# Performance work log

Measured on AMD Instinct MI355X. Metric: run time of the kernel, lower is better.

The kernel has to match this reference:

```python
import jax, jax.numpy as jnp
import numpy as np

# Model dims
B, S, D = 1, 768, 256          # batch, seq_len, d_model
H, KD = 8, 256                 # num_heads, key_dim
DH = KD // H                   # head_dim = 32
BS, NR, W, G = 64, 3, 3, 1     # block_size, num_rand_blocks, window_size, global_tokens
NEG = -1e9


def _build_sparse_indices(seed=0):
    """Replicates _create_sparse_attention_mask (sparse branch) with numpy.
    Returns (attn_indices [S, M] int32 clamped >=0, blocked_mask [1,1,S,M] float32)."""
    nb = S // BS  # num_blocks (S divisible by BS here)
    rng = np.random.RandomState(seed)
    r = np.arange(nb)
    # window pairs |i - j| <= W
    ii, jj = np.meshgrid(r, r, indexing='ij')
    win = np.abs(ii - jj) <= W
    window_pairs = np.stack([ii[win], jj[win]], axis=1)
    # global: every block -> first G blocks; first G blocks -> every block
    g = np.arange(G)
    glob_to = np.stack([np.repeat(r, G), np.tile(g, nb)], axis=1)
    glob_from = np.stack([np.repeat(g, nb), np.tile(r, G)], axis=1)
    # random pairs
    rand_pairs = rng.randint(0, nb, size=(NR * nb, 2))
    allp = np.concatenate([window_pairs, glob_to, glob_from, rand_pairs], axis=0)
    uniq = np.unique(allp[:, 0] * nb + allp[:, 1])  # sorted unique (row, col)
    rows, cols = uniq // nb, uniq % nb
    max_row = int(np.max(np.bincount(rows, minlength=nb)))
    M = max_row * BS  # padded neighbor-token width (= S when a global block is dense)
    idx = np.full((nb, M), -1, dtype=np.int64)
    for b in range(nb):
        cs = cols[rows == b]
        toks = (cs[:, None] * BS + np.arange(BS)[None, :]).reshape(-1)
        idx[b, :toks.size] = toks
    tok_idx = idx[np.arange(S) // BS]  # expand per-block rows to per-token rows [S, M]
    mask = np.where(tok_idx >= 0, 0.0, NEG).astype(np.float32)
    return np.maximum(tok_idx, 0).astype(np.int32), mask[None, None]


def setup_inputs() -> dict:
    key = jax.random.key(0)
    ks = jax.random.split(key, 8)

    def dense_w(k, fi, fo):  # glorot-uniform like keras Dense
        lim = float(np.sqrt(6.0 / (fi + fo)))
        return jax.random.uniform(k, (fi, fo), jnp.float32, -lim, lim)

    attn_indices, blocked_mask = _build_sparse_indices()
    return {
        'query': jax.random.normal(ks[0], (B, S, D), jnp.float32),
        'value': jax.random.normal(ks[1], (B, S, D), jnp.float32),
        'key_in': jax.random.normal(ks[2], (B, S, D), jnp.float32),
        'Wq': dense_w(ks[3], D, KD), 'bq': jnp.zeros((KD,), jnp.float32),
        'Wk': dense_w(ks[4], D, KD), 'bk': jnp.zeros((KD,), jnp.float32),
        'Wv': dense_w(ks[5], D, KD), 'bv': jnp.zeros((KD,), jnp.float32),
        'Wo': dense_w(ks[6], KD, D), 'bo': jnp.zeros((D,), jnp.float32),
        'attn_indices': jnp.asarray(attn_indices),
        'blocked_mask': jnp.asarray(blocked_mask),
    }


def reference(query, value, key_in, Wq, bq, Wk, bk, Wv, bv, Wo, bo, attn_indices, blocked_mask):
    q = query @ Wq + bq
    k = key_in @ Wk + bk
    v = value @ Wv + bv

    def split_heads(x):  # [B,S,KD] -> [B*H,S,DH]
        return x.reshape(B, S, H, DH).transpose(0, 2, 1, 3).reshape(B * H, S, DH)

    q = split_heads(q) * (DH ** -0.5)
    k = split_heads(k)
    v = split_heads(v)

    # gather sparse neighbor tokens (indices shared across batch*heads)
    k_g = jnp.take(k, attn_indices, axis=1)  # [BH, S, M, DH]
    v_g = jnp.take(v, attn_indices, axis=1)  # [BH, S, M, DH]

    scores = jnp.einsum('bnd,bnmd->bnm', q, k_g)  # [BH, S, M]
    M = attn_indices.shape[1]
    scores = scores.reshape(B, H, S, M) + blocked_mask  # pad positions -> -1e9
    probs = jax.nn.softmax(scores, axis=-1)

    ctx = jnp.einsum('bnm,bnmd->bnd', probs.reshape(B * H, S, M), v_g)  # [BH,S,DH]
    ctx = ctx.reshape(B, H, S, DH).transpose(0, 2, 1, 3).reshape(B, S, KD)
    out = ctx @ Wo + bo
    return out, scores, attn_indices
```

## Files before the change

### kernel.cpp

```cpp
#include <hip/hip_runtime.h>
#include <math.h>

#define SQ 768
#define DMODEL 256
#define NH 8
#define DHD 32
#define NB 12
#define QSCALE 0.1767766952966369f
#define PSHIFT 8.0f

__global__ __launch_bounds__(256) void proj3(
    const float* __restrict__ query, const float* __restrict__ value,
    const float* __restrict__ key_in,
    const float* __restrict__ Wq, const float* __restrict__ bq,
    const float* __restrict__ Wk, const float* __restrict__ bk,
    const float* __restrict__ Wv, const float* __restrict__ bv,
    const float* __restrict__ bo, float* __restrict__ outbuf,
    const int* __restrict__ aidx, float* __restrict__ idx_out,
    float* __restrict__ qhp, float* __restrict__ khp, float* __restrict__ vhp)
{
    const int j = threadIdx.x;

    {
        const int bidf = blockIdx.y * 96 + blockIdx.x;
        const int i0 = (bidf * 256 + j) * 8;
        int4 a = *(const int4*)&aidx[i0];
        int4 b = *(const int4*)&aidx[i0 + 4];
        *(float4*)&idx_out[i0] =
            make_float4((float)a.x, (float)a.y, (float)a.z, (float)a.w);
        *(float4*)&idx_out[i0 + 4] =
            make_float4((float)b.x, (float)b.y, (float)b.z, (float)b.w);
    }

    const int s0 = blockIdx.x * 8;
    const int w  = blockIdx.y;

    if (w == 0) {
        const float bb = bo[j];
        #pragma unroll
        for (int r = 0; r < 8; ++r)
            outbuf[(s0 + r) * DMODEL + j] = bb;
    }

    const float *X, *W, *bias; float* outp; float scale;
    if (w == 0)      { X = query;  W = Wq; bias = bq; outp = qhp; scale = QSCALE; }
    else if (w == 1) { X = key_in; W = Wk; bias = bk; outp = khp; scale = 1.0f; }
    else             { X = value;  W = Wv; bias = bv; outp = vhp; scale = 1.0f; }

    __shared__ __align__(16) float xs[8][DMODEL];
    __shared__ __align__(16) float ws[2][32 * DMODEL];

    {
        float* xsf = &xs[0][0];
        const float* Xp = X + s0 * DMODEL;
        const int i0 = j * 8;
        *(float4*)&xsf[i0]     = *(const float4*)&Xp[i0];
        *(float4*)&xsf[i0 + 4] = *(const float4*)&Xp[i0 + 4];

        #pragma unroll
        for (int t = 0; t < 8; ++t)
            *(float4*)&ws[0][t * 1024 + j * 4] =
                *(const float4*)&W[t * 1024 + j * 4];
    }
    __syncthreads();

    const int j0 = (j & 63) * 4;
    const int r0 = (j >> 6) * 2;

    float4 acc0 = make_float4(0.f, 0.f, 0.f, 0.f);
    float4 acc1 = make_float4(0.f, 0.f, 0.f, 0.f);
    int cur = 0;

    for (int c = 0; c < 8; ++c) {
        float4 wreg[8];
        if (c < 7) {
            const float* Wc = W + (c + 1) * 8192;
            #pragma unroll
            for (int t = 0; t < 8; ++t)
                wreg[t] = *(const float4*)&Wc[t * 1024 + j * 4];
        }

        const float* wb = &ws[cur][0];
        #pragma unroll
        for (int k4 = 0; k4 < 8; ++k4) {
            const int kb = c * 32 + k4 * 4;
            float4 x0 = *(const float4*)&xs[r0 + 0][kb];
            float4 x1 = *(const float4*)&xs[r0 + 1][kb];
            float4 w0 = *(const float4*)&wb[(k4 * 4 + 0) * DMODEL + j0];
            float4 w1 = *(const float4*)&wb[(k4 * 4 + 1) * DMODEL + j0];
            float4 w2 = *(const float4*)&wb[(k4 * 4 + 2) * DMODEL + j0];
            float4 w3 = *(const float4*)&wb[(k4 * 4 + 3) * DMODEL + j0];
            acc0.x = fmaf(x0.x, w0.x, acc0.x); acc0.y = fmaf(x0.x, w0.y, acc0.y);
            acc0.z = fmaf(x0.x, w0.z, acc0.z); acc0.w = fmaf(x0.x, w0.w, acc0.w);
            acc0.x = fmaf(x0.y, w1.x, acc0.x); acc0.y = fmaf(x0.y, w1.y, acc0.y);
            acc0.z = fmaf(x0.y, w1.z, acc0.z); acc0.w = fmaf(x0.y, w1.w, acc0.w);
            acc0.x = fmaf(x0.z, w2.x, acc0.x); acc0.y = fmaf(x0.z, w2.y, acc0.y);
            acc0.z = fmaf(x0.z, w2.z, acc0.z); acc0.w = fmaf(x0.z, w2.w, acc0.w);
            acc0.x = fmaf(x0.w, w3.x, acc0.x); acc0.y = fmaf(x0.w, w3.y, acc0.y);
            acc0.z = fmaf(x0.w, w3.z, acc0.z); acc0.w = fmaf(x0.w, w3.w, acc0.w);
            acc1.x = fmaf(x1.x, w0.x, acc1.x); acc1.y = fmaf(x1.x, w0.y, acc1.y);
            acc1.z = fmaf(x1.x, w0.z, acc1.z); acc1.w = fmaf(x1.x, w0.w, acc1.w);
            acc1.x = fmaf(x1.y, w1.x, acc1.x); acc1.y = fmaf(x1.y, w1.y, acc1.y);
            acc1.z = fmaf(x1.y, w1.z, acc1.z); acc1.w = fmaf(x1.y, w1.w, acc1.w);
            acc1.x = fmaf(x1.z, w2.x, acc1.x); acc1.y = fmaf(x1.z, w2.y, acc1.y);
            acc1.z = fmaf(x1.z, w2.z, acc1.z); acc1.w = fmaf(x1.z, w2.w, acc1.w);
            acc1.x = fmaf(x1.w, w3.x, acc1.x); acc1.y = fmaf(x1.w, w3.y, acc1.y);
            acc1.z = fmaf(x1.w, w3.z, acc1.z); acc1.w = fmaf(x1.w, w3.w, acc1.w);
        }

        if (c < 7) {
            float* wd = &ws[cur ^ 1][0];
            #pragma unroll
            for (int t = 0; t < 8; ++t)
                *(float4*)&wd[t * 1024 + j * 4] = wreg[t];
            __syncthreads();
            cur ^= 1;
        }
    }

    const float4 bb = *(const float4*)&bias[j0];
    const int h = j0 >> 5, d = j0 & 31;
    {
        float4 o0, o1;
        o0.x = (acc0.x + bb.x) * scale; o0.y = (acc0.y + bb.y) * scale;
        o0.z = (acc0.z + bb.z) * scale; o0.w = (acc0.w + bb.w) * scale;
        o1.x = (acc1.x + bb.x) * scale; o1.y = (acc1.y + bb.y) * scale;
        o1.z = (acc1.z + bb.z) * scale; o1.w = (acc1.w + bb.w) * scale;
        *(float4*)&outp[h * (SQ * DHD) + (s0 + r0 + 0) * DHD + d] = o0;
        *(float4*)&outp[h * (SQ * DHD) + (s0 + r0 + 1) * DHD + d] = o1;
    }
}

__global__ __launch_bounds__(512) void attn2(
    const float* __restrict__ qh, const float* __restrict__ kh,
    const float* __restrict__ vh, const int* __restrict__ aidx,
    const float* __restrict__ mask, const float* __restrict__ Wo,
    float* __restrict__ scores_out, float* __restrict__ out, int M)
{
    __shared__ __align__(16) float Ks[2][2][32][68];
    __shared__ __align__(16) float Vs[2][2][64][36];
    __shared__ __align__(16) float Ps[2][32][68];
    __shared__ float dot0s[32];
    __shared__ float invL[32];

    const int b    = blockIdx.x;
    const int half = blockIdx.y;
    const int h    = blockIdx.z;
    const int s0b  = b * 64;
    const int s0   = s0b + half * 32;
    const int tid  = threadIdx.x;
    const int u    = tid >> 8;
    const int utid = tid & 255;
    const int NCH2 = M / 128;

    const int qrt = (utid & 15) * 2;
    const int qct = (utid >> 4) * 4;
    const int rp  = utid & 15;
    const int dg  = (utid >> 4) & 3;
    const int cg  = utid >> 6;
    const int c   = utid & 63;
    const int sg  = utid >> 6;
    const int d4a = sg * 4;
    const int d4b = 16 + sg * 4;

    const float* mrow = &mask[s0b * M];
    const int*   arow = &aidx[s0b * M];
    float*       srow = &scores_out[(h * SQ + s0) * M];

    float qr0[32], qr1[32];
    {
        const float* qp = &qh[(h * SQ + s0 + qrt) * DHD];
        #pragma unroll
        for (int d4 = 0; d4 < DHD; d4 += 4) {
            float4 a  = *(const float4*)&qp[d4];
            float4 b4 = *(const float4*)&qp[DHD + d4];
            qr0[d4] = a.x;  qr0[d4+1] = a.y;  qr0[d4+2] = a.z;  qr0[d4+3] = a.w;
            qr1[d4] = b4.x; qr1[d4+1] = b4.y; qr1[d4+2] = b4.z; qr1[d4+3] = b4.w;
        }
    }

    if (tid < 16) {
        const float* k0 = &kh[h * SQ * DHD];
        float a0 = 0.f, a1 = 0.f;
        #pragma unroll
        for (int d = 0; d < DHD; ++d) {
            const float kv = k0[d];
            a0 = fmaf(qr0[d], kv, a0);
            a1 = fmaf(qr1[d], kv, a1);
        }
        dot0s[qrt] = a0; dot0s[qrt + 1] = a1;
    }

    float mv_cur = mrow[(u * NCH2) * 64];
    bool  val_cur = mv_cur > -0.5f;
    if (val_cur) {
        const int t0 = arow[(u * NCH2) * 64];
        const float* kp = &kh[(h * SQ + t0 + c) * DHD];
        const float* vp = &vh[(h * SQ + t0 + c) * DHD];
        float4 ka = *(const float4*)&kp[d4a];
        float4 kb = *(const float4*)&kp[d4b];
        Ks[u][0][d4a+0][c] = ka.x; Ks[u][0][d4a+1][c] = ka.y;
        Ks[u][0][d4a+2][c] = ka.z; Ks[u][0][d4a+3][c] = ka.w;
        Ks[u][0][d4b+0][c] = kb.x; Ks[u][0][d4b+1][c] = kb.y;
        Ks[u][0][d4b+2][c] = kb.z; Ks[u][0][d4b+3][c] = kb.w;
        *(float4*)&Vs[u][0][c][d4a] = *(const float4*)&vp[d4a];
        *(float4*)&Vs[u][0][c][d4b] = *(const float4*)&vp[d4b];
    }
    __syncthreads();

    float4 acc0a = make_float4(0.f,0.f,0.f,0.f), acc0b = acc0a;
    float4 acc1a = acc0a, acc1b = acc0a;
    float rps0 = 0.f, rps1 = 0.f;
    int cur = 0;

    for (int ci = 0; ci < NCH2; ++ci) {
        const int m0 = (u * NCH2 + ci) * 64;

        bool  val_nxt = false;
        float mv_nxt  = 0.f;
        float4 ka, kb, va, vb;
        if (ci + 1 < NCH2) {
            mv_nxt  = mrow[m0 + 64];
            val_nxt = mv_nxt > -0.5f;
            if (val_nxt) {
                const int t0 = arow[m0 + 64];
                const float* kp = &kh[(h * SQ + t0 + c) * DHD];
                const float* vp = &vh[(h * SQ + t0 + c) * DHD];
                ka = *(const float4*)&kp[d4a];
                kb = *(const float4*)&kp[d4b];
                va = *(const float4*)&vp[d4a];
                vb = *(const float4*)&vp[d4b];
            }
        }

        if (val_cur) {
            const float* Kb = &Ks[u][cur][0][qct];
            float sc[2][4] = {};
            #pragma unroll
            for (int kk = 0; kk < 32; ++kk) {
                float4 b4 = *(const float4*)&Kb[kk * 68];
                sc[0][0] = fmaf(qr0[kk], b4.x, sc[0][0]);
                sc[0][1] = fmaf(qr0[kk], b4.y, sc[0][1]);
                sc[0][2] = fmaf(qr0[kk], b4.z, sc[0][2]);
                sc[0][3] = fmaf(qr0[kk], b4.w, sc[0][3]);
                sc[1][0] = fmaf(qr1[kk], b4.x, sc[1][0]);
                sc[1][1] = fmaf(qr1[kk], b4.y, sc[1][1]);
                sc[1][2] = fmaf(qr1[kk], b4.z, sc[1][2]);
                sc[1][3] = fmaf(qr1[kk], b4.w, sc[1][3]);
            }
            {
                *(float4*)&srow[(qrt + 0) * M + m0 + qct] =
                    make_float4(sc[0][0], sc[0][1], sc[0][2], sc[0][3]);
                float4 e;
                e.x = __expf(sc[0][0] - PSHIFT); e.y = __expf(sc[0][1] - PSHIFT);
                e.z = __expf(sc[0][2] - PSHIFT); e.w = __expf(sc[0][3] - PSHIFT);
                *(float4*)&Ps[u][qrt + 0][qct] = e;
                rps0 += (e.x + e.y) + (e.z + e.w);
            }
            {
                *(float4*)&srow[(qrt + 1) * M + m0 + qct] =
                    make_float4(sc[1][0], sc[1][1], sc[1][2], sc[1][3]);
                float4 e;
                e.x = __expf(sc[1][0] - PSHIFT); e.y = __expf(sc[1][1] - PSHIFT);
                e.z = __expf(sc[1][2] - PSHIFT); e.w = __expf(sc[1][3] - PSHIFT);
                *(float4*)&Ps[u][qrt + 1][qct] = e;
                rps1 += (e.x + e.y) + (e.z + e.w);
            }
        } else {
            #pragma unroll
            for (int i = 0; i < 8; ++i) {
                const int e = utid + i * 256;
                const int r = e >> 6, cc = e & 63;
                srow[r * M + m0 + cc] = dot0s[r] + mv_cur;
            }
        }

        if (val_nxt) {
            Ks[u][cur^1][d4a+0][c] = ka.x; Ks[u][cur^1][d4a+1][c] = ka.y;
            Ks[u][cur^1][d4a+2][c] = ka.z; Ks[u][cur^1][d4a+3][c] = ka.w;
            Ks[u][cur^1][d4b+0][c] = kb.x; Ks[u][cur^1][d4b+1][c] = kb.y;
            Ks[u][cur^1][d4b+2][c] = kb.z; Ks[u][cur^1][d4b+3][c] = kb.w;
            *(float4*)&Vs[u][cur^1][c][d4a] = va;
            *(float4*)&Vs[u][cur^1][c][d4b] = vb;
        }
        __syncthreads();

        if (val_cur) {
            const float (*Vb)[36] = Vs[u][cur];
            const float* Pr0 = &Ps[u][2 * rp][0];
            const float* Pr1 = &Ps[u][2 * rp + 1][0];
            const int c0 = cg * 16;
            const int dd = dg * 8;
            #pragma unroll
            for (int k = 0; k < 4; ++k) {
                float4 pa = *(const float4*)&Pr0[c0 + k * 4];
                float4 pb = *(const float4*)&Pr1[c0 + k * 4];
                const float pav[4] = {pa.x, pa.y, pa.z, pa.w};
                const float pbv[4] = {pb.x, pb.y, pb.z, pb.w};
                #pragma unroll
                for (int t = 0; t < 4; ++t) {
                    const int cc2 = c0 + k * 4 + t;
                    float4 v0 = *(const float4*)&Vb[cc2][dd];
                    float4 v1 = *(const float4*)&Vb[cc2][dd + 4];
                    acc0a.x = fmaf(pav[t], v0.x, acc0a.x);
                    acc0a.y = fmaf(pav[t], v0.y, acc0a.y);
                    acc0a.z = fmaf(pav[t], v0.z, acc0a.z);
                    acc0a.w = fmaf(pav[t], v0.w, acc0a.w);
                    acc0b.x = fmaf(pav[t], v1.x, acc0b.x);
                    acc0b.y = fmaf(pav[t], v1.y, acc0b.y);
                    acc0b.z = fmaf(pav[t], v1.z, acc0b.z);
                    acc0b.w = fmaf(pav[t], v1.w, acc0b.w);
                    acc1a.x = fmaf(pbv[t], v0.x, acc1a.x);
                    acc1a.y = fmaf(pbv[t], v0.y, acc1a.y);
                    acc1a.z = fmaf(pbv[t], v0.z, acc1a.z);
                    acc1a.w = fmaf(pbv[t], v0.w, acc1a.w);
                    acc1b.x = fmaf(pbv[t], v1.x, acc1b.x);
                    acc1b.y = fmaf(pbv[t], v1.y, acc1b.y);
                    acc1b.z = fmaf(pbv[t], v1.z, acc1b.z);
                    acc1b.w = fmaf(pbv[t], v1.w, acc1b.w);
                }
            }
        }
        __syncthreads();

        val_cur = val_nxt; mv_cur = mv_nxt; cur ^= 1;
    }

    float* vacc = &Vs[0][0][0][0];
    float* rsum = &Ps[0][0][0];
    {
        const int s = u * 4 + cg;
        float* base = vacc + (s * 32 + 2 * rp) * 36 + dg * 8;
        *(float4*)&base[0]  = acc0a; *(float4*)&base[4]  = acc0b;
        *(float4*)&base[36] = acc1a; *(float4*)&base[40] = acc1b;
        const int qg = utid >> 4;
        rsum[(u * 16 + qg) * 32 + qrt]     = rps0;
        rsum[(u * 16 + qg) * 32 + qrt + 1] = rps1;
    }
    __syncthreads();

    if (tid < 32) {
        float pt = 0.f;
        #pragma unroll
        for (int s2 = 0; s2 < 32; ++s2) pt += rsum[s2 * 32 + tid];
        invL[tid] = 1.0f / pt;
    }
    __syncthreads();

    float* ctxn = &Ks[0][0][0][0];
    if (tid < 256) {
        const int r = tid & 31, dq = tid >> 5;
        float4 sum = make_float4(0.f, 0.f, 0.f, 0.f);
        #pragma unroll
        for (int s = 0; s < 8; ++s) {
            float4 v = *(const float4*)&vacc[(s * 32 + r) * 36 + dq * 4];
            sum.x += v.x; sum.y += v.y; sum.z += v.z; sum.w += v.w;
        }
        const float il = invL[r];
        sum.x *= il; sum.y *= il; sum.z *= il; sum.w *= il;
        *(float4*)&ctxn[r * 36 + dq * 4] = sum;
    }
    __syncthreads();

    {
        const int jc = tid & 255, rg = tid >> 8;
        float wo[32];
        #pragma unroll
        for (int k = 0; k < 32; ++k)
            wo[k] = Wo[(h * DHD + k) * DMODEL + jc];
        for (int rr = rg * 16; rr < rg * 16 + 16; ++rr) {
            float a = 0.f;
            #pragma unroll
            for (int k4 = 0; k4 < 8; ++k4) {
                float4 cv = *(const float4*)&ctxn[rr * 36 + k4 * 4];
                a = fmaf(cv.x, wo[k4 * 4 + 0], a);
                a = fmaf(cv.y, wo[k4 * 4 + 1], a);
                a = fmaf(cv.z, wo[k4 * 4 + 2], a);
                a = fmaf(cv.w, wo[k4 * 4 + 3], a);
            }
            atomicAdd(&out[(s0 + rr) * DMODEL + jc], a);
        }
    }
}

extern "C" void kernel_launch(void* const* d_in, const int* in_sizes, int n_in,
                              void* d_out, int out_size, void* d_ws, size_t ws_size,
                              hipStream_t stream)
{
    const float* query  = (const float*)d_in[0];
    const float* value  = (const float*)d_in[1];
    const float* key_in = (const float*)d_in[2];
    const float* Wq = (const float*)d_in[3];
    const float* bq = (const float*)d_in[4];
    const float* Wk = (const float*)d_in[5];
    const float* bk = (const float*)d_in[6];
    const float* Wv = (const float*)d_in[7];
    const float* bv = (const float*)d_in[8];
    const float* Wo = (const float*)d_in[9];
    const float* bo = (const float*)d_in[10];
    const int*   aidx = (const int*)d_in[11];
    const float* mask = (const float*)d_in[12];

    const int M = in_sizes[11] / SQ;

    float* out        = (float*)d_out;
    float* scores_out = out + SQ * DMODEL;
    float* idx_out    = scores_out + NH * SQ * M;

    float* ws  = (float*)d_ws;
    float* qhp = ws;
    float* khp = qhp + NH * SQ * DHD;
    float* vhp = khp + NH * SQ * DHD;

    proj3<<<dim3(96, 3), 256, 0, stream>>>(
        query, value, key_in, Wq, bq, Wk, bk, Wv, bv,
        bo, out, aidx, idx_out, qhp, khp, vhp);

    attn2<<<dim3(NB, 2, NH), 512, 0, stream>>>(
        qhp, khp, vhp, aidx, mask, Wo, scores_out, out, M);
}
```

Baseline: 48.88 us.

## Fuse P·V into the score loop using transposed V and register accumulators

V tiles are now stored transposed in shared memory, and each thread multiplies its own exponentiated scores by V right after computing them. This drops the shared-memory probability buffer and one block barrier per chunk. Partial context sums are then reduced across lanes with warp shuffles before the final cross-wave reduction. In exchange each thread holds 64 float accumulators plus the q registers, which raises register pressure and may lower occupancy. The transposed V stores are scalar writes.

```diff
diff --git a/kernel.cpp b/kernel.cpp
--- a/kernel.cpp
+++ b/kernel.cpp
@@ -138,8 +138,7 @@
     float* __restrict__ scores_out, float* __restrict__ out, int M)
 {
     __shared__ __align__(16) float Ks[2][2][32][68];
-    __shared__ __align__(16) float Vs[2][2][64][36];
-    __shared__ __align__(16) float Ps[2][32][68];
+    __shared__ __align__(16) float Vt[2][2][32][68];
     __shared__ float dot0s[32];
     __shared__ float invL[32];
 
@@ -155,9 +154,6 @@
 
     const int qrt = (utid & 15) * 2;
     const int qct = (utid >> 4) * 4;
-    const int rp  = utid & 15;
-    const int dg  = (utid >> 4) & 3;
-    const int cg  = utid >> 6;
     const int c   = utid & 63;
     const int sg  = utid >> 6;
     const int d4a = sg * 4;
@@ -199,17 +195,22 @@
         const float* vp = &vh[(h * SQ + t0 + c) * DHD];
         float4 ka = *(const float4*)&kp[d4a];
         float4 kb = *(const float4*)&kp[d4b];
+        float4 va = *(const float4*)&vp[d4a];
+        float4 vb = *(const float4*)&vp[d4b];
         Ks[u][0][d4a+0][c] = ka.x; Ks[u][0][d4a+1][c] = ka.y;
         Ks[u][0][d4a+2][c] = ka.z; Ks[u][0][d4a+3][c] = ka.w;
         Ks[u][0][d4b+0][c] = kb.x; Ks[u][0][d4b+1][c] = kb.y;
         Ks[u][0][d4b+2][c] = kb.z; Ks[u][0][d4b+3][c] = kb.w;
-        *(float4*)&Vs[u][0][c][d4a] = *(const float4*)&vp[d4a];
-        *(float4*)&Vs[u][0][c][d4b] = *(const float4*)&vp[d4b];
+        Vt[u][0][d4a+0][c] = va.x; Vt[u][0][d4a+1][c] = va.y;
+        Vt[u][0][d4a+2][c] = va.z; Vt[u][0][d4a+3][c] = va.w;
+        Vt[u][0][d4b+0][c] = vb.x; Vt[u][0][d4b+1][c] = vb.y;
+        Vt[u][0][d4b+2][c] = vb.z; Vt[u][0][d4b+3][c] = vb.w;
     }
     __syncthreads();
 
-    float4 acc0a = make_float4(0.f,0.f,0.f,0.f), acc0b = acc0a;
-    float4 acc1a = acc0a, acc1b = acc0a;
+    float a0s[32], a1s[32];
+    #pragma unroll
+    for (int d = 0; d < 32; ++d) { a0s[d] = 0.f; a1s[d] = 0.f; }
     float rps0 = 0.f, rps1 = 0.f;
     int cur = 0;
 
@@ -248,23 +249,27 @@
                 sc[1][2] = fmaf(qr1[kk], b4.z, sc[1][2]);
                 sc[1][3] = fmaf(qr1[kk], b4.w, sc[1][3]);
             }
-            {
-                *(float4*)&srow[(qrt + 0) * M + m0 + qct] =
-                    make_float4(sc[0][0], sc[0][1], sc[0][2], sc[0][3]);
-                float4 e;
-                e.x = __expf(sc[0][0] - PSHIFT); e.y = __expf(sc[0][1] - PSHIFT);
-                e.z = __expf(sc[0][2] - PSHIFT); e.w = __expf(sc[0][3] - PSHIFT);
-                *(float4*)&Ps[u][qrt + 0][qct] = e;
-                rps0 += (e.x + e.y) + (e.z + e.w);
-            }
-            {
-                *(float4*)&srow[(qrt + 1) * M + m0 + qct] =
-                    make_float4(sc[1][0], sc[1][1], sc[1][2], sc[1][3]);
-                float4 e;
-                e.x = __expf(sc[1][0] - PSHIFT); e.y = __expf(sc[1][1] - PSHIFT);
-                e.z = __expf(sc[1][2] - PSHIFT); e.w = __expf(sc[1][3] - PSHIFT);
-                *(float4*)&Ps[u][qrt + 1][qct] = e;
-                rps1 += (e.x + e.y) + (e.z + e.w);
+            *(float4*)&srow[(qrt + 0) * M + m0 + qct] =
+                make_float4(sc[0][0], sc[0][1], sc[0][2], sc[0][3]);
+            *(float4*)&srow[(qrt + 1) * M + m0 + qct] =
+                make_float4(sc[1][0], sc[1][1], sc[1][2], sc[1][3]);
+            float e0[4], e1[4];
+            #pragma unroll
+            for (int t = 0; t < 4; ++t) {
+                e0[t] = __expf(sc[0][t] - PSHIFT);
+                e1[t] = __expf(sc[1][t] - PSHIFT);
+            }
+            rps0 += (e0[0] + e0[1]) + (e0[2] + e0[3]);
+            rps1 += (e1[0] + e1[1]) + (e1[2] + e1[3]);
+
+            const float* Vb = &Vt[u][cur][0][qct];
+            #pragma unroll
+            for (int d = 0; d < 32; ++d) {
+                float4 v = *(const float4*)&Vb[d * 68];
+                a0s[d] = fmaf(e0[0], v.x, fmaf(e0[1], v.y,
+                         fmaf(e0[2], v.z, fmaf(e0[3], v.w, a0s[d]))));
+                a1s[d] = fmaf(e1[0], v.x, fmaf(e1[1], v.y,
+                         fmaf(e1[2], v.z, fmaf(e1[3], v.w, a1s[d]))));
             }
         } else {
             #pragma unroll
@@ -280,74 +285,53 @@
             Ks[u][cur^1][d4a+2][c] = ka.z; Ks[u][cur^1][d4a+3][c] = ka.w;
             Ks[u][cur^1][d4b+0][c] = kb.x; Ks[u][cur^1][d4b+1][c] = kb.y;
             Ks[u][cur^1][d4b+2][c] = kb.z; Ks[u][cur^1][d4b+3][c] = kb.w;
-            *(float4*)&Vs[u][cur^1][c][d4a] = va;
-            *(float4*)&Vs[u][cur^1][c][d4b] = vb;
+            Vt[u][cur^1][d4a+0][c] = va.x; Vt[u][cur^1][d4a+1][c] = va.y;
+            Vt[u][cur^1][d4a+2][c] = va.z; Vt[u][cur^1][d4a+3][c] = va.w;
+            Vt[u][cur^1][d4b+0][c] = vb.x; Vt[u][cur^1][d4b+1][c] = vb.y;
+            Vt[u][cur^1][d4b+2][c] = vb.z; Vt[u][cur^1][d4b+3][c] = vb.w;
         }
         __syncthreads();
 
-        if (val_cur) {
-            const float (*Vb)[36] = Vs[u][cur];
-            const float* Pr0 = &Ps[u][2 * rp][0];
-            const float* Pr1 = &Ps[u][2 * rp + 1][0];
-            const int c0 = cg * 16;
-            const int dd = dg * 8;
-            #pragma unroll
-            for (int k = 0; k < 4; ++k) {
-                float4 pa = *(const float4*)&Pr0[c0 + k * 4];
-                float4 pb = *(const float4*)&Pr1[c0 + k * 4];
-                const float pav[4] = {pa.x, pa.y, pa.z, pa.w};
-                const float pbv[4] = {pb.x, pb.y, pb.z, pb.w};
-                #pragma unroll
-                for (int t = 0; t < 4; ++t) {
-                    const int cc2 = c0 + k * 4 + t;
-                    float4 v0 = *(const float4*)&Vb[cc2][dd];
-                    float4 v1 = *(const float4*)&Vb[cc2][dd + 4];
-                    acc0a.x = fmaf(pav[t], v0.x, acc0a.x);
-                    acc0a.y = fmaf(pav[t], v0.y, acc0a.y);
-                    acc0a.z = fmaf(pav[t], v0.z, acc0a.z);
-                    acc0a.w = fmaf(pav[t], v0.w, acc0a.w);
-                    acc0b.x = fmaf(pav[t], v1.x, acc0b.x);
-                    acc0b.y = fmaf(pav[t], v1.y, acc0b.y);
-                    acc0b.z = fmaf(pav[t], v1.z, acc0b.z);
-                    acc0b.w = fmaf(pav[t], v1.w, acc0b.w);
-                    acc1a.x = fmaf(pbv[t], v0.x, acc1a.x);
-                    acc1a.y = fmaf(pbv[t], v0.y, acc1a.y);
-                    acc1a.z = fmaf(pbv[t], v0.z, acc1a.z);
-                    acc1a.w = fmaf(pbv[t], v0.w, acc1a.w);
-                    acc1b.x = fmaf(pbv[t], v1.x, acc1b.x);
-                    acc1b.y = fmaf(pbv[t], v1.y, acc1b.y);
-                    acc1b.z = fmaf(pbv[t], v1.z, acc1b.z);
-                    acc1b.w = fmaf(pbv[t], v1.w, acc1b.w);
-                }
-            }
-        }
-        __syncthreads();
-
         val_cur = val_nxt; mv_cur = mv_nxt; cur ^= 1;
     }
 
-    float* vacc = &Vs[0][0][0][0];
-    float* rsum = &Ps[0][0][0];
-    {
-        const int s = u * 4 + cg;
-        float* base = vacc + (s * 32 + 2 * rp) * 36 + dg * 8;
-        *(float4*)&base[0]  = acc0a; *(float4*)&base[4]  = acc0b;
-        *(float4*)&base[36] = acc1a; *(float4*)&base[40] = acc1b;
-        const int qg = utid >> 4;
-        rsum[(u * 16 + qg) * 32 + qrt]     = rps0;
-        rsum[(u * 16 + qg) * 32 + qrt + 1] = rps1;
+    #pragma unroll
+    for (int d = 0; d < 32; ++d) {
+        a0s[d] += __shfl_xor(a0s[d], 16);
+        a0s[d] += __shfl_xor(a0s[d], 32);
+        a1s[d] += __shfl_xor(a1s[d], 16);
+        a1s[d] += __shfl_xor(a1s[d], 32);
+    }
+    rps0 += __shfl_xor(rps0, 16); rps0 += __shfl_xor(rps0, 32);
+    rps1 += __shfl_xor(rps1, 16); rps1 += __shfl_xor(rps1, 32);
+
+    float* vacc = &Ks[0][0][0][0];
+    float* rsum = vacc + 8 * 32 * 36;
+    const int wv = tid >> 6, lane = tid & 63;
+    if (lane < 16) {
+        const int rp2 = lane * 2;
+        float* base0 = vacc + (wv * 32 + rp2) * 36;
+        #pragma unroll
+        for (int dq = 0; dq < 8; ++dq) {
+            *(float4*)&base0[dq * 4] =
+                make_float4(a0s[dq*4+0], a0s[dq*4+1], a0s[dq*4+2], a0s[dq*4+3]);
+            *(float4*)&base0[36 + dq * 4] =
+                make_float4(a1s[dq*4+0], a1s[dq*4+1], a1s[dq*4+2], a1s[dq*4+3]);
+        }
+        rsum[wv * 32 + rp2]     = rps0;
+        rsum[wv * 32 + rp2 + 1] = rps1;
     }
     __syncthreads();
 
     if (tid < 32) {
         float pt = 0.f;
         #pragma unroll
-        for (int s2 = 0; s2 < 32; ++s2) pt += rsum[s2 * 32 + tid];
+        for (int s2 = 0; s2 < 8; ++s2) pt += rsum[s2 * 32 + tid];
         invL[tid] = 1.0f / pt;
     }
     __syncthreads();
 
-    float* ctxn = &Ks[0][0][0][0];
+    float* ctxn = &Vt[0][0][0][0];
     if (tid < 256) {
         const int r = tid & 31, dq = tid >> 5;
         float4 sum = make_float4(0.f, 0.f, 0.f, 0.f);
```

New measurement: 60.04 us. +22.8%, slower.

## Retile PV accumulation to 4x8 per thread with wave-shuffle reduction

Applied to the files above, without the earlier changes.

The probability-times-V loop is remapped so each thread accumulates 4 query rows by 8 head dims over 8 columns, instead of 2 rows over 16 columns. This raises register reuse of the loaded V values and cuts shared-memory reads per FMA. Partial sums from the two half-waves are combined with a cross-lane shuffle before the existing shared-memory reduction. A launch-bounds occupancy hint of 2 blocks is also added, which may constrain registers and risk spills with the doubled accumulator count.

```diff
diff --git a/kernel.cpp b/kernel.cpp
--- a/kernel.cpp
+++ b/kernel.cpp
@@ -131,7 +131,7 @@
     }
 }
 
-__global__ __launch_bounds__(512) void attn2(
+__global__ __launch_bounds__(512, 2) void attn2(
     const float* __restrict__ qh, const float* __restrict__ kh,
     const float* __restrict__ vh, const int* __restrict__ aidx,
     const float* __restrict__ mask, const float* __restrict__ Wo,
@@ -155,9 +155,9 @@
 
     const int qrt = (utid & 15) * 2;
     const int qct = (utid >> 4) * 4;
-    const int rp  = utid & 15;
-    const int dg  = (utid >> 4) & 3;
-    const int cg  = utid >> 6;
+    const int rq  = utid & 7;
+    const int dgp = (utid >> 3) & 3;
+    const int cgp = utid >> 5;
     const int c   = utid & 63;
     const int sg  = utid >> 6;
     const int d4a = sg * 4;
@@ -208,8 +208,12 @@
     }
     __syncthreads();
 
-    float4 acc0a = make_float4(0.f,0.f,0.f,0.f), acc0b = acc0a;
-    float4 acc1a = acc0a, acc1b = acc0a;
+    float4 accA[4], accB[4];
+    #pragma unroll
+    for (int i = 0; i < 4; ++i) {
+        accA[i] = make_float4(0.f, 0.f, 0.f, 0.f);
+        accB[i] = make_float4(0.f, 0.f, 0.f, 0.f);
+    }
     float rps0 = 0.f, rps1 = 0.f;
     int cur = 0;
 
@@ -287,52 +291,69 @@
 
         if (val_cur) {
             const float (*Vb)[36] = Vs[u][cur];
-            const float* Pr0 = &Ps[u][2 * rp][0];
-            const float* Pr1 = &Ps[u][2 * rp + 1][0];
-            const int c0 = cg * 16;
-            const int dd = dg * 8;
-            #pragma unroll
-            for (int k = 0; k < 4; ++k) {
-                float4 pa = *(const float4*)&Pr0[c0 + k * 4];
-                float4 pb = *(const float4*)&Pr1[c0 + k * 4];
-                const float pav[4] = {pa.x, pa.y, pa.z, pa.w};
-                const float pbv[4] = {pb.x, pb.y, pb.z, pb.w};
+            const int r0q = rq * 4;
+            const int c0 = cgp * 8;
+            const int dd = dgp * 8;
+            #pragma unroll
+            for (int k = 0; k < 2; ++k) {
+                float4 p0 = *(const float4*)&Ps[u][r0q + 0][c0 + k * 4];
+                float4 p1 = *(const float4*)&Ps[u][r0q + 1][c0 + k * 4];
+                float4 p2 = *(const float4*)&Ps[u][r0q + 2][c0 + k * 4];
+                float4 p3 = *(const float4*)&Ps[u][r0q + 3][c0 + k * 4];
+                const float pv[4][4] = {
+                    {p0.x, p0.y, p0.z, p0.w}, {p1.x, p1.y, p1.z, p1.w},
+                    {p2.x, p2.y, p2.z, p2.w}, {p3.x, p3.y, p3.z, p3.w}};
                 #pragma unroll
                 for (int t = 0; t < 4; ++t) {
                     const int cc2 = c0 + k * 4 + t;
                     float4 v0 = *(const float4*)&Vb[cc2][dd];
                     float4 v1 = *(const float4*)&Vb[cc2][dd + 4];
-                    acc0a.x = fmaf(pav[t], v0.x, acc0a.x);
-                    acc0a.y = fmaf(pav[t], v0.y, acc0a.y);
-                    acc0a.z = fmaf(pav[t], v0.z, acc0a.z);
-                    acc0a.w = fmaf(pav[t], v0.w, acc0a.w);
-                    acc0b.x = fmaf(pav[t], v1.x, acc0b.x);
-                    acc0b.y = fmaf(pav[t], v1.y, acc0b.y);
-                    acc0b.z = fmaf(pav[t], v1.z, acc0b.z);
-                    acc0b.w = fmaf(pav[t], v1.w, acc0b.w);
-                    acc1a.x = fmaf(pbv[t], v0.x, acc1a.x);
-                    acc1a.y = fmaf(pbv[t], v0.y, acc1a.y);
-                    acc1a.z = fmaf(pbv[t], v0.z, acc1a.z);
-                    acc1a.w = fmaf(pbv[t], v0.w, acc1a.w);
-                    acc1b.x = fmaf(pbv[t], v1.x, acc1b.x);
-                    acc1b.y = fmaf(pbv[t], v1.y, acc1b.y);
-                    acc1b.z = fmaf(pbv[t], v1.z, acc1b.z);
-                    acc1b.w = fmaf(pbv[t], v1.w, acc1b.w);
+                    #pragma unroll
+                    for (int i = 0; i < 4; ++i) {
+                        accA[i].x = fmaf(pv[i][t], v0.x, accA[i].x);
+                        accA[i].y = fmaf(pv[i][t], v0.y, accA[i].y);
+                        accA[i].z = fmaf(pv[i][t], v0.z, accA[i].z);
+                        accA[i].w = fmaf(pv[i][t], v0.w, accA[i].w);
+                        accB[i].x = fmaf(pv[i][t], v1.x, accB[i].x);
+                        accB[i].y = fmaf(pv[i][t], v1.y, accB[i].y);
+                        accB[i].z = fmaf(pv[i][t], v1.z, accB[i].z);
+                        accB[i].w = fmaf(pv[i][t], v1.w, accB[i].w);
+                    }
                 }
             }
         }
         __syncthreads();
 
         val_cur = val_nxt; mv_cur = mv_nxt; cur ^= 1;
+    }
+
+    #pragma unroll
+    for (int i = 0; i < 4; ++i) {
+        accA[i].x += __shfl_xor(accA[i].x, 32);
+        accA[i].y += __shfl_xor(accA[i].y, 32);
+        accA[i].z += __shfl_xor(accA[i].z, 32);
+        accA[i].w += __shfl_xor(accA[i].w, 32);
+        accB[i].x += __shfl_xor(accB[i].x, 32);
+        accB[i].y += __shfl_xor(accB[i].y, 32);
+        accB[i].z += __shfl_xor(accB[i].z, 32);
+        accB[i].w += __shfl_xor(accB[i].w, 32);
     }
 
     float* vacc = &Vs[0][0][0][0];
     float* rsum = &Ps[0][0][0];
     {
-        const int s = u * 4 + cg;
-        float* base = vacc + (s * 32 + 2 * rp) * 36 + dg * 8;
-        *(float4*)&base[0]  = acc0a; *(float4*)&base[4]  = acc0b;
-        *(float4*)&base[36] = acc1a; *(float4*)&base[40] = acc1b;
+        const int lane = tid & 63;
+        if (lane < 32) {
+            const int s = u * 4 + (utid >> 6);
+            const int rr0 = (lane & 7) * 4;
+            const int ddw = ((lane >> 3) & 3) * 8;
+            float* base = vacc + (s * 32 + rr0) * 36 + ddw;
+            #pragma unroll
+            for (int i = 0; i < 4; ++i) {
+                *(float4*)&base[i * 36 + 0] = accA[i];
+                *(float4*)&base[i * 36 + 4] = accB[i];
+            }
+        }
         const int qg = utid >> 4;
         rsum[(u * 16 + qg) * 32 + qrt]     = rps0;
         rsum[(u * 16 + qg) * 32 + qrt + 1] = rps1;
```

Result: slower. 57.56 us (+17.8%).
